# Optimization experiments

Hardware: AMD Instinct MI355X
Metric: run time of the kernel (lower is better)

Reference implementation:

```python
import jax, jax.numpy as jnp
import numpy as np

EPS = 2e-05
N_H_RDG = 9   # lifting scale grid: h_j = 2**j, j=0..8
N_H_CROP = 3  # group-conv scale support: offsets 0,1,2 (dyadic index shifts)


def _scaled_kernel(w, h):
    """Resample base kernel w [O, I, K] (taps on integers centered at 0) at
    coordinates x/h via linear interpolation -> [O, I, (K-1)*h+1], with the
    R+ Haar-measure normalization 1/h (psi_h(x) = psi(x/h)/h)."""
    K = w.shape[-1]
    Kh = (K - 1) * h + 1
    m = jnp.arange(K, dtype=jnp.float32) - K // 2
    x = (jnp.arange(Kh, dtype=jnp.float32) - Kh // 2) / h
    hat = jnp.maximum(0.0, 1.0 - jnp.abs(x[:, None] - m[None, :]))  # [Kh, K]
    return jnp.einsum('oim,xm->oix', w, hat) / h


def _conv1d_same(x, k):
    pad = (k.shape[-1] - 1) // 2
    return jax.lax.conv_general_dilated(
        x, k, window_strides=(1,), padding=[(pad, pad)],
        dimension_numbers=('NCH', 'OIH', 'NCH'))


def _pool_r1(x, stride):
    # max pool over the spatial (last) axis only: kernel 4, pad 1 each side
    return jax.lax.reduce_window(
        x, -jnp.inf, jax.lax.max,
        window_dimensions=(1, 1, 1, 4), window_strides=(1, 1, 1, stride),
        padding=((0, 0), (0, 0), (0, 0), (1, 1)))


def _bn(x, g, b):
    # BatchNorm2d over [B, C, H_scale, L], training-mode batch stats
    mu = jnp.mean(x, axis=(0, 2, 3), keepdims=True)
    var = jnp.var(x, axis=(0, 2, 3), keepdims=True)
    return (x - mu) * jax.lax.rsqrt(var + EPS) * g[None, :, None, None] + b[None, :, None, None]


def _forward(x, w1, w2, w3, g1, b1, g2, b2, g3, b3, fw1, fb1, fw2, fb2, fw3, fb3):
    B = x.shape[0]
    # --- c1: GConvRdG lifting, scales h_j = 2**j, j=0..8 ---
    out = jnp.stack([_conv1d_same(x, _scaled_kernel(w1, 2 ** j))
                     for j in range(N_H_RDG)], axis=2)      # [B,16,9,16]
    out = _bn(jax.nn.relu(_pool_r1(out, 2)), g1, b1)        # [B,16,9,8]
    # --- c2: GConvGG, h_crop=True: out scale j uses in scales j..j+2 ---
    O2, I2 = w2.shape[0], w2.shape[1]
    w2r = w2.reshape(O2, I2 * N_H_CROP, 3)
    H2 = out.shape[2] - (N_H_CROP - 1)  # 7
    out = jnp.stack([
        _conv1d_same(out[:, :, j:j + N_H_CROP, :].reshape(B, I2 * N_H_CROP, -1),
                     _scaled_kernel(w2r, 2 ** j))
        for j in range(H2)], axis=2)                        # [B,32,7,8]
    out = _bn(jax.nn.relu(_pool_r1(out, 2)), g2, b2)        # [B,32,7,4]
    # --- c3: GConvGG with 1x1 spatial kernel ---
    w3s = w3[:, :, :, 0]  # [64,32,3]
    H3 = out.shape[2] - (N_H_CROP - 1)  # 5
    out = jnp.stack([
        jnp.einsum('oik,bikl->bol', w3s, out[:, :, j:j + N_H_CROP, :]) / (2.0 ** j)
        for j in range(H3)], axis=2)                        # [B,64,5,4]
    out = _bn(jax.nn.relu(_pool_r1(out, 4)), g3, b3)        # [B,64,5,1]
    # --- MLP head (dropout is identity in eval) ---
    out = out.reshape(B, -1)                                # [B,320]
    out = out @ fw1.T + fb1
    out = out @ fw2.T + fb2
    return out @ fw3.T + fb3                                # [B,17]


def setup_inputs() -> dict:
    key = jax.random.key(0)
    ks = jax.random.split(key, 7)
    B = 4096
    x = jax.random.normal(ks[0], (B, 6, 16), dtype=jnp.float32)
    w1 = jax.random.normal(ks[1], (16, 6, 7), dtype=jnp.float32) * (6 * 7) ** -0.5
    w2 = jax.random.normal(ks[2], (32, 16, 3, 3), dtype=jnp.float32) * (16 * 3 * 3) ** -0.5
    w3 = jax.random.normal(ks[3], (64, 32, 3, 1), dtype=jnp.float32) * (32 * 3) ** -0.5
    fw1 = jax.random.normal(ks[4], (16, 320), dtype=jnp.float32) * 320 ** -0.5
    fw2 = jax.random.normal(ks[5], (16, 16), dtype=jnp.float32) * 16 ** -0.5
    fw3 = jax.random.normal(ks[6], (17, 16), dtype=jnp.float32) * 16 ** -0.5
    return {
        'x': x, 'w1': w1, 'w2': w2, 'w3': w3,
        'g1': jnp.ones(16), 'b1': jnp.zeros(16),
        'g2': jnp.ones(32), 'b2': jnp.zeros(32),
        'g3': jnp.ones(64), 'b3': jnp.zeros(64),
        'fw1': fw1, 'fb1': jnp.zeros(16),
        'fw2': fw2, 'fb2': jnp.zeros(16),
        'fw3': fw3, 'fb3': jnp.zeros(17),
    }


def reference(x, w1, w2, w3, g1, b1, g2, b2, g3, b3, fw1, fb1, fw2, fb2, fw3, fb3):
    return _forward(x, w1, w2, w3, g1, b1, g2, b2, g3, b3, fw1, fb1, fw2, fb2, fw3, fb3)
```

## Files before the change

kernel.cpp:

```cpp
#include <hip/hip_runtime.h>

#define EPS 2e-5f

using short8  = __attribute__((ext_vector_type(8))) short;
using floatx4 = __attribute__((ext_vector_type(4))) float;

static __device__ inline unsigned short f2bf(float f) {
    unsigned u = __float_as_uint(f);
    u += 0x7fffu + ((u >> 16) & 1u);
    return (unsigned short)(u >> 16);
}


__global__ void __launch_bounds__(256) k_setup(const float* __restrict__ w1,
                                               unsigned short* __restrict__ W1f,
                                               float* __restrict__ stats) {
    int gid = blockIdx.x * 256 + threadIdx.x;
    if (gid < 256) stats[gid] = 0.f;
    if (gid >= 221184) return;
    int j  = gid / 24576;
    int r  = gid % 24576;
    int T  = r / 1536;
    int r2 = r % 1536;
    int ks = r2 / 512;
    int r3 = r2 % 512;
    int lane = r3 >> 3, e = r3 & 7;
    int n  = T * 16 + (lane & 15);
    int kk = ks * 32 + (lane >> 4) * 8 + e;
    int o = n >> 4, t = n & 15;
    int i = kk >> 4, s = kk & 15;
    int h = 1 << j;
    int d = s - t;
    float val = 0.f;
    if (d >= -3 * h && d <= 3 * h) {
        float df = (float)d / (float)h;
        #pragma unroll
        for (int m = 0; m < 7; ++m) {
            float hat = fmaxf(0.f, 1.f - fabsf(df - (float)(m - 3)));
            val += w1[(o * 6 + i) * 7 + m] * hat;
        }
        val /= (float)h;
    }
    W1f[gid] = f2bf(val);
}

__global__ void __launch_bounds__(256) k1(const float* __restrict__ x,
                                          const unsigned short* __restrict__ W1f,
                                          unsigned short* __restrict__ p1,
                                          float* __restrict__ stats1) {
    int j    = blockIdx.y;
    int wav  = threadIdx.x >> 6;
    int lane = threadIdx.x & 63;
    int msub = wav & 1, nh = wav >> 1;
    int mt   = blockIdx.x * 2 + msub;
    int quad = lane >> 4, l15 = lane & 15;
    floatx4 z = {0.f, 0.f, 0.f, 0.f};
    floatx4 acc[8];
    #pragma unroll
    for (int T = 0; T < 8; ++T) acc[T] = z;
    const float* xr = x + (size_t)(mt * 16 + l15) * 96;
    const short8* Bj = (const short8*)W1f + (size_t)(j * 16) * 3 * 64;
    #pragma unroll
    for (int ks = 0; ks < 3; ++ks) {
        int k0 = ks * 32 + quad * 8;
        floatx4 v0 = *(const floatx4*)(xr + k0);
        floatx4 v1 = *(const floatx4*)(xr + k0 + 4);
        short8 a;
        #pragma unroll
        for (int e = 0; e < 4; ++e) {
            a[e]     = (short)f2bf(v0[e]);
            a[e + 4] = (short)f2bf(v1[e]);
        }
        #pragma unroll
        for (int T = 0; T < 8; ++T) {
            short8 b = Bj[((nh * 8 + T) * 3 + ks) * 64 + lane];
            acc[T] = __builtin_amdgcn_mfma_f32_16x16x32_bf16(a, b, acc[T], 0, 0, 0);
        }
    }
    __shared__ float ls[32];
    if (threadIdx.x < 32) ls[threadIdx.x] = 0.f;
    __syncthreads();
    int mbase = mt * 16 + quad * 4;
    int tp = l15;
    bool act = tp < 8;
    int tpe = tp & 7;
    int base = lane & 48;
    int c0 = base + max(2 * tpe - 1, 0);
    int c1 = base + 2 * tpe;
    int c2 = base + 2 * tpe + 1;
    int c3 = base + min(2 * tpe + 2, 15);
    #pragma unroll
    for (int T = 0; T < 8; ++T) {
        int o = nh * 8 + T;
        float psum = 0.f, pss = 0.f;
        #pragma unroll
        for (int r = 0; r < 4; ++r) {
            float v  = acc[T][r];
            float mx = fmaxf(fmaxf(__shfl(v, c0, 64), __shfl(v, c1, 64)),
                             fmaxf(__shfl(v, c2, 64), __shfl(v, c3, 64)));
            mx = fmaxf(mx, 0.f);
            if (act) {
                p1[(size_t)(mbase + r) * 1152 + o * 72 + j * 8 + tp] = f2bf(mx);
                psum += mx; pss += mx * mx;
            }
        }
        #pragma unroll
        for (int m = 32; m >= 1; m >>= 1) {
            psum += __shfl_xor(psum, m, 64);
            pss  += __shfl_xor(pss,  m, 64);
        }
        if (lane == 0) {
            atomicAdd(&ls[o], psum);
            atomicAdd(&ls[16 + o], pss);
        }
    }
    __syncthreads();
    if (threadIdx.x < 16) {
        atomicAdd(&stats1[threadIdx.x], ls[threadIdx.x]);
        atomicAdd(&stats1[16 + threadIdx.x], ls[16 + threadIdx.x]);
    }
}

__global__ void __launch_bounds__(384) k_bias(const float* __restrict__ w2,
                                              const float* __restrict__ g1,
                                              const float* __restrict__ b1,
                                              const float* __restrict__ stats1,
                                              unsigned short* __restrict__ W2f,
                                              float* __restrict__ bias2,
                                              float invN1) {
    int blk = blockIdx.x;
    int j   = blk >> 8;
    int col = blk & 255;
    int o = col >> 3, t = col & 7;
    int k = threadIdx.x;
    int ic = k >> 3, s = k & 7;
    int i = ic / 3, c = ic % 3;
    float mu  = stats1[i] * invN1;
    float var = stats1[16 + i] * invN1 - mu * mu;
    float rsg = rsqrtf(var + EPS);
    float a1  = g1[i] * rsg;
    float d1  = b1[i] - mu * a1;
    int h = 1 << j;
    int d = s - t;
    float raw = 0.f;
    if (d >= -h && d <= h) {
        float df = (float)d / (float)h;
        #pragma unroll
        for (int m = 0; m < 3; ++m) {
            float hat = fmaxf(0.f, 1.f - fabsf(df - (float)(m - 1)));
            raw += w2[((o * 16 + i) * 3 + c) * 3 + m] * hat;
        }
        raw /= (float)h;
    }
    {
        int T    = col >> 4;
        int lane = (col & 15) + ((k >> 3) & 3) * 16;
        int ks   = k >> 5;
        int e    = k & 7;
        W2f[(((size_t)(j * 16 + T) * 12 + ks) * 64 + lane) * 8 + e] = f2bf(raw * a1);
    }
    __shared__ float red[384];
    red[k] = raw * d1;
    __syncthreads();
    if (k < 128) red[k] += red[k + 128] + red[k + 256];
    __syncthreads();
    for (int st = 64; st >= 1; st >>= 1) {
        if (k < st) red[k] += red[k + st];
        __syncthreads();
    }
    if (k == 0) bias2[j * 256 + col] = red[0];
}

__global__ void __launch_bounds__(256) k2(const unsigned short* __restrict__ p1,
                                          const unsigned short* __restrict__ W2f,
                                          const float* __restrict__ bias2,
                                          unsigned short* __restrict__ p2s,
                                          float* __restrict__ stats2,
                                          int B) {
    int j    = blockIdx.y;
    int wav  = threadIdx.x >> 6;
    int lane = threadIdx.x & 63;
    int nh   = wav & 1, mp = wav >> 1;
    int m0   = blockIdx.x * 64 + mp * 32;
    int quad = lane >> 4, l15 = lane & 15;
    floatx4 z = {0.f, 0.f, 0.f, 0.f};
    floatx4 acc[2][8];
    #pragma unroll
    for (int mi = 0; mi < 2; ++mi)
        #pragma unroll
        for (int T = 0; T < 8; ++T) acc[mi][T] = z;
    const short8* Bj = (const short8*)W2f + (size_t)(j * 16) * 12 * 64;
    const unsigned short* Arow0 = p1 + (size_t)(m0 + l15) * 1152;
    const unsigned short* Arow1 = Arow0 + 16 * 1152;
    #pragma unroll
    for (int ks = 0; ks < 12; ++ks) {
        int k0 = ks * 32 + quad * 8;
        int i  = k0 / 24;
        int c  = (k0 - i * 24) >> 3;
        int off = i * 72 + (j + c) * 8;
        short8 a0 = *(const short8*)(Arow0 + off);
        short8 a1 = *(const short8*)(Arow1 + off);
        #pragma unroll
        for (int T = 0; T < 8; ++T) {
            short8 b = Bj[((nh * 8 + T) * 12 + ks) * 64 + lane];
            acc[0][T] = __builtin_amdgcn_mfma_f32_16x16x32_bf16(a0, b, acc[0][T], 0, 0, 0);
            acc[1][T] = __builtin_amdgcn_mfma_f32_16x16x32_bf16(a1, b, acc[1][T], 0, 0, 0);
        }
    }
    __shared__ float ls[64];
    if (threadIdx.x < 64) ls[threadIdx.x] = 0.f;
    __syncthreads();
    int tp  = lane & 7;
    bool act = tp < 4;
    int tpe = tp & 3;
    int base = lane & 56;
    int c0 = base + max(2 * tpe - 1, 0);
    int c1 = base + 2 * tpe;
    int c2 = base + 2 * tpe + 1;
    int c3 = base + min(2 * tpe + 2, 7);
    #pragma unroll
    for (int T = 0; T < 8; ++T) {
        int n = (nh * 8 + T) * 16 + l15;
        int o = n >> 3;
        float bias = bias2[j * 256 + n];
        float psum = 0.f, pss = 0.f;
        #pragma unroll
        for (int mi = 0; mi < 2; ++mi) {
            int mbase = m0 + mi * 16 + quad * 4;
            #pragma unroll
            for (int r = 0; r < 4; ++r) {
                float v  = acc[mi][T][r] + bias;
                float mx = fmaxf(fmaxf(__shfl(v, c0, 64), __shfl(v, c1, 64)),
                                 fmaxf(__shfl(v, c2, 64), __shfl(v, c3, 64)));
                mx = fmaxf(mx, 0.f);
                if (act) {
                    p2s[(((size_t)j * 4 + tp) * B + mbase + r) * 32 + o] = f2bf(mx);
                    psum += mx; pss += mx * mx;
                }
            }
        }
        #pragma unroll
        for (int m = 0; m < 5; ++m) {
            int msk = (m < 3) ? (1 << m) : (1 << (m + 1));
            psum += __shfl_xor(psum, msk, 64);
            pss  += __shfl_xor(pss,  msk, 64);
        }
        if (lane == 0 || lane == 8) {
            int oo = (nh * 8 + T) * 2 + (lane >> 3);
            atomicAdd(&ls[oo], psum);
            atomicAdd(&ls[32 + oo], pss);
        }
    }
    __syncthreads();
    if (threadIdx.x < 32) {
        atomicAdd(&stats2[threadIdx.x], ls[threadIdx.x]);
        atomicAdd(&stats2[32 + threadIdx.x], ls[32 + threadIdx.x]);
    }
}

__global__ void __launch_bounds__(256) k3(const unsigned short* __restrict__ p2s,
                                          const float* __restrict__ w3,
                                          const float* __restrict__ g2,
                                          const float* __restrict__ b2,
                                          const float* __restrict__ stats2,
                                          float* __restrict__ act3,
                                          float* __restrict__ stats3,
                                          float invN2, int B) {
    int j    = blockIdx.y;
    int wav  = threadIdx.x >> 6;
    int lane = threadIdx.x & 63;
    int msub = wav & 1, nh = wav >> 1;
    int m0   = (blockIdx.x * 2 + msub) * 16;
    int quad = lane >> 4, l15 = lane & 15;
    __shared__ float a2s[32], d2s[32], bias3s[64], ls[128];
    __shared__ unsigned short W3s[6144];
    if (threadIdx.x < 128) ls[threadIdx.x] = 0.f;
    if (threadIdx.x < 32) {
        int i = threadIdx.x;
        float mu  = stats2[i] * invN2;
        float var = stats2[32 + i] * invN2 - mu * mu;
        float rsg = rsqrtf(var + EPS);
        a2s[i] = g2[i] * rsg;
        d2s[i] = b2[i] - mu * a2s[i];
    }
    __syncthreads();
    for (int idx = threadIdx.x; idx < 6144; idx += 256) {
        int e  = idx & 7;
        int ln = (idx >> 3) & 63;
        int fs = idx >> 9;
        int Tg = fs / 3, ks = fs % 3;
        int n = Tg * 16 + (ln & 15);
        int i = (ln >> 4) * 8 + e;
        W3s[idx] = f2bf(w3[n * 96 + i * 3 + ks] * a2s[i]);
    }
    if (threadIdx.x < 64) {
        float s = 0.f;
        for (int i = 0; i < 32; ++i)
            #pragma unroll
            for (int kk = 0; kk < 3; ++kk)
                s = fmaf(w3[threadIdx.x * 96 + i * 3 + kk], d2s[i], s);
        bias3s[threadIdx.x] = s;
    }
    __syncthreads();
    short8 bf[2][3];
    #pragma unroll
    for (int T = 0; T < 2; ++T)
        #pragma unroll
        for (int ks = 0; ks < 3; ++ks)
            bf[T][ks] = *(const short8*)&W3s[(((nh * 2 + T) * 3 + ks) * 64 + lane) * 8];
    floatx4 z = {0.f, 0.f, 0.f, 0.f};
    floatx4 acc[2][3];
    #pragma unroll
    for (int T = 0; T < 2; ++T)
        #pragma unroll
        for (int l = 0; l < 3; ++l) acc[T][l] = z;
    #pragma unroll
    for (int ks = 0; ks < 3; ++ks) {
        int jj = j + ks;
        #pragma unroll
        for (int l = 0; l < 3; ++l) {
            const short8* ap =
                (const short8*)(p2s + ((size_t)(jj * 4 + l) * B + m0 + l15) * 32) + quad;
            short8 a = *ap;
            #pragma unroll
            for (int T = 0; T < 2; ++T)
                acc[T][l] = __builtin_amdgcn_mfma_f32_16x16x32_bf16(a, bf[T][ks],
                                                                    acc[T][l], 0, 0, 0);
        }
    }
    float inv = 1.f / (float)(1 << j);
    int mbase = m0 + quad * 4;
    #pragma unroll
    for (int T = 0; T < 2; ++T) {
        int col = nh * 32 + T * 16 + l15;
        float bias = bias3s[col];
        float psum = 0.f, pss = 0.f;
        #pragma unroll
        for (int r = 0; r < 4; ++r) {
            float v = fmaxf(fmaxf(acc[T][0][r], acc[T][1][r]), acc[T][2][r]);
            v = fmaxf((v + bias) * inv, 0.f);
            act3[(size_t)(mbase + r) * 320 + col * 5 + j] = v;
            psum += v; pss += v * v;
        }
        psum += __shfl_xor(psum, 16, 64); pss += __shfl_xor(pss, 16, 64);
        psum += __shfl_xor(psum, 32, 64); pss += __shfl_xor(pss, 32, 64);
        if (quad == 0) {
            atomicAdd(&ls[col], psum);
            atomicAdd(&ls[64 + col], pss);
        }
    }
    __syncthreads();
    if (threadIdx.x < 64) {
        atomicAdd(&stats3[threadIdx.x], ls[threadIdx.x]);
        atomicAdd(&stats3[64 + threadIdx.x], ls[64 + threadIdx.x]);
    }
}

__global__ void __launch_bounds__(128) k4(const float* __restrict__ act3,
                                          const float* __restrict__ g3,
                                          const float* __restrict__ b3,
                                          const float* __restrict__ stats3,
                                          const float* __restrict__ fw1,
                                          const float* __restrict__ fb1,
                                          const float* __restrict__ fw2,
                                          const float* __restrict__ fb2,
                                          const float* __restrict__ fw3,
                                          const float* __restrict__ fb3,
                                          float* __restrict__ out,
                                          float invN3) {
    __shared__ float a3s[64], d3s[64];
    __shared__ unsigned short W1s[5120];
    __shared__ float fw2s[256], fw3s[272], fb2s[16], fb3s[17], fb1f[16];
    __shared__ float hbuf[2][16][17];
    int tid = threadIdx.x;
    if (tid < 64) {
        float mu  = stats3[tid] * invN3;
        float var = stats3[64 + tid] * invN3 - mu * mu;
        float rsg = rsqrtf(var + EPS);
        a3s[tid] = g3[tid] * rsg;
        d3s[tid] = b3[tid] - mu * a3s[tid];
    }
    __syncthreads();
    for (int idx = tid; idx < 5120; idx += 128) {
        int e  = idx & 7;
        int ln = (idx >> 3) & 63;
        int ks = idx >> 9;
        int n  = ln & 15;
        int k  = ks * 32 + (ln >> 4) * 8 + e;
        W1s[idx] = f2bf(fw1[n * 320 + k] * a3s[k / 5]);
    }
    for (int idx = tid; idx < 256; idx += 128) fw2s[idx] = fw2[idx];
    for (int idx = tid; idx < 272; idx += 128) fw3s[idx] = fw3[idx];
    if (tid < 16) fb2s[tid] = fb2[tid];
    if (tid < 17) fb3s[tid] = fb3[tid];
    if (tid < 16) {
        float s = fb1[tid];
        for (int o = 0; o < 64; ++o) {
            float dd = d3s[o];
            #pragma unroll
            for (int jj = 0; jj < 5; ++jj)
                s = fmaf(fw1[tid * 320 + o * 5 + jj], dd, s);
        }
        fb1f[tid] = s;
    }
    __syncthreads();
    int wav = tid >> 6, lane = tid & 63;
    int quad = lane >> 4, l15 = lane & 15;
    int mt = blockIdx.x * 2 + wav;
    const float* ar = act3 + (size_t)(mt * 16 + l15) * 320;
    floatx4 acc = {0.f, 0.f, 0.f, 0.f};
    #pragma unroll
    for (int ks = 0; ks < 10; ++ks) {
        int k0 = ks * 32 + quad * 8;
        floatx4 v0 = *(const floatx4*)(ar + k0);
        floatx4 v1 = *(const floatx4*)(ar + k0 + 4);
        short8 a;
        #pragma unroll
        for (int e = 0; e < 4; ++e) {
            a[e]     = (short)f2bf(v0[e]);
            a[e + 4] = (short)f2bf(v1[e]);
        }
        short8 b = *(const short8*)&W1s[(ks * 64 + lane) * 8];
        acc = __builtin_amdgcn_mfma_f32_16x16x32_bf16(a, b, acc, 0, 0, 0);
    }
    #pragma unroll
    for (int r = 0; r < 4; ++r)
        hbuf[wav][quad * 4 + r][l15] = acc[r] + fb1f[l15];
    __syncthreads();
    if (lane < 16) {
        int row = l15;
        float hv[16];
        #pragma unroll
        for (int n = 0; n < 16; ++n) hv[n] = hbuf[wav][row][n];
        float h2[16];
        #pragma unroll
        for (int f2 = 0; f2 < 16; ++f2) {
            float s = fb2s[f2];
            #pragma unroll
            for (int n = 0; n < 16; ++n) s = fmaf(fw2s[f2 * 16 + n], hv[n], s);
            h2[f2] = s;
        }
        float* orow = out + (size_t)(mt * 16 + row) * 17;
        #pragma unroll
        for (int f3 = 0; f3 < 17; ++f3) {
            float s = fb3s[f3];
            #pragma unroll
            for (int n = 0; n < 16; ++n) s = fmaf(fw3s[f3 * 16 + n], h2[n], s);
            orow[f3] = s;
        }
    }
}

extern "C" void kernel_launch(void* const* d_in, const int* in_sizes, int n_in,
                              void* d_out, int out_size, void* d_ws, size_t ws_size,
                              hipStream_t stream) {
    (void)n_in; (void)out_size; (void)ws_size;
    const float* x   = (const float*)d_in[0];
    const float* w1  = (const float*)d_in[1];
    const float* w2  = (const float*)d_in[2];
    const float* w3  = (const float*)d_in[3];
    const float* g1  = (const float*)d_in[4];
    const float* b1  = (const float*)d_in[5];
    const float* g2  = (const float*)d_in[6];
    const float* b2  = (const float*)d_in[7];
    const float* g3  = (const float*)d_in[8];
    const float* b3  = (const float*)d_in[9];
    const float* fw1 = (const float*)d_in[10];
    const float* fb1 = (const float*)d_in[11];
    const float* fw2 = (const float*)d_in[12];
    const float* fb2 = (const float*)d_in[13];
    const float* fw3 = (const float*)d_in[14];
    const float* fb3 = (const float*)d_in[15];
    float* out = (float*)d_out;

    int B = in_sizes[0] / 96;

    char* wsb = (char*)d_ws;
    float*          stats  = (float*)wsb;
    unsigned short* W1f    = (unsigned short*)(wsb + 1024);
    unsigned short* W2f    = W1f + 221184;
    float*          bias2  = (float*)(W2f + 688128);
    unsigned short* p1     = (unsigned short*)(bias2 + 1792);
    unsigned short* p2s    = p1 + (size_t)B * 1152;
    float*          act3   = (float*)(p2s + (size_t)B * 896);

    float* stats1 = stats;
    float* stats2 = stats + 32;
    float* stats3 = stats + 96;

    float invN1 = 1.f / (float)(B * 72);
    float invN2 = 1.f / (float)(B * 28);
    float invN3 = 1.f / (float)(B * 5);

    k_setup<<<864, 256, 0, stream>>>(w1, W1f, stats);
    k1<<<dim3(B / 32, 9), 256, 0, stream>>>(x, W1f, p1, stats1);
    k_bias<<<7 * 256, 384, 0, stream>>>(w2, g1, b1, stats1, W2f, bias2, invN1);
    k2<<<dim3(B / 64, 7), 256, 0, stream>>>(p1, W2f, bias2, p2s, stats2, B);
    k3<<<dim3(B / 32, 5), 256, 0, stream>>>(p2s, w3, g2, b2, stats2, act3, stats3,
                                            invN2, B);
    k4<<<B / 32, 128, 0, stream>>>(act3, g3, b3, stats3, fw1, fb1, fw2, fb2, fw3, fb3,
                                   out, invN3);
}
```

Baseline: 204.1 us.

## Restage epilogues through shared memory and re-layout intermediates for vector stores

The per-element shuffle pooling and scattered 2-byte global stores in k1/k2 are replaced by staging MFMA accumulators in LDS, doing the max-pool per thread, and writing packed short8 rows. The p1, p2s and act3 intermediates get scale-major layouts, with act3 now stored as bf16 instead of fp32. k3 is restructured so the BN-folded weights become the A operand and are built in registers rather than staged in LDS. k4 runs at 16 rows per 64-thread block and reads the bf16 act3 directly. The aim is to cut global memory traffic and uncoalesced stores, at the cost of more LDS use and extra barriers.

```diff
diff --git a/kernel.cpp b/kernel.cpp
--- a/kernel.cpp
+++ b/kernel.cpp
@@ -12,9 +12,9 @@
 }
 
 
-__global__ void __launch_bounds__(256) k_setup(const float* __restrict__ w1,
-                                               unsigned short* __restrict__ W1f,
-                                               float* __restrict__ stats) {
+__global__ void __launch_bounds__(256) kS(const float* __restrict__ w1,
+                                          unsigned short* __restrict__ W1f,
+                                          float* __restrict__ stats) {
     int gid = blockIdx.x * 256 + threadIdx.x;
     if (gid < 256) stats[gid] = 0.f;
     if (gid >= 221184) return;
@@ -24,9 +24,9 @@
     int r2 = r % 1536;
     int ks = r2 / 512;
     int r3 = r2 % 512;
-    int lane = r3 >> 3, e = r3 & 7;
-    int n  = T * 16 + (lane & 15);
-    int kk = ks * 32 + (lane >> 4) * 8 + e;
+    int ln = r3 >> 3, e = r3 & 7;
+    int n  = T * 16 + (ln & 15);
+    int kk = ks * 32 + (ln >> 4) * 8 + e;
     int o = n >> 4, t = n & 15;
     int i = kk >> 4, s = kk & 15;
     int h = 1 << j;
@@ -47,18 +47,18 @@
 __global__ void __launch_bounds__(256) k1(const float* __restrict__ x,
                                           const unsigned short* __restrict__ W1f,
                                           unsigned short* __restrict__ p1,
-                                          float* __restrict__ stats1) {
-    int j    = blockIdx.y;
-    int wav  = threadIdx.x >> 6;
-    int lane = threadIdx.x & 63;
+                                          float* __restrict__ stats1, int B) {
+    __shared__ float z[32 * 276];
+    __shared__ float lsS[256], lsQ[256];
+    int tid = threadIdx.x, j = blockIdx.y;
+    int wav = tid >> 6, lane = tid & 63;
+    int quad = lane >> 4, l15 = lane & 15;
     int msub = wav & 1, nh = wav >> 1;
-    int mt   = blockIdx.x * 2 + msub;
-    int quad = lane >> 4, l15 = lane & 15;
-    floatx4 z = {0.f, 0.f, 0.f, 0.f};
+    int b0 = blockIdx.x * 32;
     floatx4 acc[8];
     #pragma unroll
-    for (int T = 0; T < 8; ++T) acc[T] = z;
-    const float* xr = x + (size_t)(mt * 16 + l15) * 96;
+    for (int T = 0; T < 8; ++T) acc[T] = floatx4{0.f, 0.f, 0.f, 0.f};
+    const float* xr = x + (size_t)(b0 + msub * 16 + l15) * 96;
     const short8* Bj = (const short8*)W1f + (size_t)(j * 16) * 3 * 64;
     #pragma unroll
     for (int ks = 0; ks < 3; ++ks) {
@@ -77,47 +77,49 @@
             acc[T] = __builtin_amdgcn_mfma_f32_16x16x32_bf16(a, b, acc[T], 0, 0, 0);
         }
     }
-    __shared__ float ls[32];
-    if (threadIdx.x < 32) ls[threadIdx.x] = 0.f;
-    __syncthreads();
-    int mbase = mt * 16 + quad * 4;
-    int tp = l15;
-    bool act = tp < 8;
-    int tpe = tp & 7;
-    int base = lane & 48;
-    int c0 = base + max(2 * tpe - 1, 0);
-    int c1 = base + 2 * tpe;
-    int c2 = base + 2 * tpe + 1;
-    int c3 = base + min(2 * tpe + 2, 15);
     #pragma unroll
     for (int T = 0; T < 8; ++T) {
-        int o = nh * 8 + T;
-        float psum = 0.f, pss = 0.f;
-        #pragma unroll
-        for (int r = 0; r < 4; ++r) {
-            float v  = acc[T][r];
-            float mx = fmaxf(fmaxf(__shfl(v, c0, 64), __shfl(v, c1, 64)),
-                             fmaxf(__shfl(v, c2, 64), __shfl(v, c3, 64)));
-            mx = fmaxf(mx, 0.f);
-            if (act) {
-                p1[(size_t)(mbase + r) * 1152 + o * 72 + j * 8 + tp] = f2bf(mx);
-                psum += mx; pss += mx * mx;
-            }
-        }
-        #pragma unroll
-        for (int m = 32; m >= 1; m >>= 1) {
-            psum += __shfl_xor(psum, m, 64);
-            pss  += __shfl_xor(pss,  m, 64);
-        }
-        if (lane == 0) {
-            atomicAdd(&ls[o], psum);
-            atomicAdd(&ls[16 + o], pss);
-        }
-    }
-    __syncthreads();
-    if (threadIdx.x < 16) {
-        atomicAdd(&stats1[threadIdx.x], ls[threadIdx.x]);
-        atomicAdd(&stats1[16 + threadIdx.x], ls[16 + threadIdx.x]);
+        int col = (nh * 8 + T) * 16 + l15;
+        int rb  = msub * 16 + quad * 4;
+        #pragma unroll
+        for (int r = 0; r < 4; ++r) z[(rb + r) * 276 + col] = acc[T][r];
+    }
+    __syncthreads();
+    float psum = 0.f, pss = 0.f;
+    #pragma unroll
+    for (int i = 0; i < 2; ++i) {
+        int u = tid + 256 * i;
+        int row = u >> 4, o = u & 15;
+        const float* zr = &z[row * 276 + o * 16];
+        floatx4 q0 = ((const floatx4*)zr)[0];
+        floatx4 q1 = ((const floatx4*)zr)[1];
+        floatx4 q2 = ((const floatx4*)zr)[2];
+        floatx4 q3 = ((const floatx4*)zr)[3];
+        float t[16] = {q0[0], q0[1], q0[2], q0[3], q1[0], q1[1], q1[2], q1[3],
+                       q2[0], q2[1], q2[2], q2[3], q3[0], q3[1], q3[2], q3[3]};
+        short8 pk;
+        #pragma unroll
+        for (int tp = 0; tp < 8; ++tp) {
+            int lo = (tp == 0) ? 0 : 2 * tp - 1;
+            int hi = (tp == 7) ? 15 : 2 * tp + 2;
+            float m = t[lo];
+            for (int tt = lo + 1; tt <= hi; ++tt) m = fmaxf(m, t[tt]);
+            m = fmaxf(m, 0.f);
+            pk[tp] = (short)f2bf(m);
+            psum += m; pss += m * m;
+        }
+        *(short8*)(p1 + ((size_t)j * B + b0 + row) * 128 + o * 8) = pk;
+    }
+    lsS[(tid & 15) * 16 + (tid >> 4)] = psum;
+    lsQ[(tid & 15) * 16 + (tid >> 4)] = pss;
+    __syncthreads();
+    if (tid < 32) {
+        int o = tid & 15;
+        const float* src = (tid < 16) ? lsS : lsQ;
+        float s = 0.f;
+        #pragma unroll
+        for (int g = 0; g < 16; ++g) s += src[o * 16 + g];
+        atomicAdd(&stats1[(tid < 16 ? 0 : 16) + o], s);
     }
 }
 
@@ -175,31 +177,28 @@
                                           const unsigned short* __restrict__ W2f,
                                           const float* __restrict__ bias2,
                                           unsigned short* __restrict__ p2s,
-                                          float* __restrict__ stats2,
-                                          int B) {
-    int j    = blockIdx.y;
-    int wav  = threadIdx.x >> 6;
-    int lane = threadIdx.x & 63;
-    int nh   = wav & 1, mp = wav >> 1;
-    int m0   = blockIdx.x * 64 + mp * 32;
+                                          float* __restrict__ stats2, int B) {
+    __shared__ float z[32 * 260];
+    __shared__ unsigned short pt[4][64][40];
+    __shared__ float lsS[512], lsQ[512];
+    int tid = threadIdx.x, j = blockIdx.y;
+    int wav = tid >> 6, lane = tid & 63;
     int quad = lane >> 4, l15 = lane & 15;
-    floatx4 z = {0.f, 0.f, 0.f, 0.f};
+    int nh = wav & 1, mp = wav >> 1;
+    int b0 = blockIdx.x * 64, m0 = b0 + mp * 32;
     floatx4 acc[2][8];
     #pragma unroll
     for (int mi = 0; mi < 2; ++mi)
         #pragma unroll
-        for (int T = 0; T < 8; ++T) acc[mi][T] = z;
+        for (int T = 0; T < 8; ++T) acc[mi][T] = floatx4{0.f, 0.f, 0.f, 0.f};
     const short8* Bj = (const short8*)W2f + (size_t)(j * 16) * 12 * 64;
-    const unsigned short* Arow0 = p1 + (size_t)(m0 + l15) * 1152;
-    const unsigned short* Arow1 = Arow0 + 16 * 1152;
     #pragma unroll
     for (int ks = 0; ks < 12; ++ks) {
-        int k0 = ks * 32 + quad * 8;
-        int i  = k0 / 24;
-        int c  = (k0 - i * 24) >> 3;
-        int off = i * 72 + (j + c) * 8;
-        short8 a0 = *(const short8*)(Arow0 + off);
-        short8 a1 = *(const short8*)(Arow1 + off);
+        int icq = ks * 4 + quad;
+        int i = icq / 3, c = icq - i * 3;
+        const unsigned short* ap = p1 + ((size_t)(j + c) * B + m0 + l15) * 128 + i * 8;
+        short8 a0 = *(const short8*)ap;
+        short8 a1 = *(const short8*)(ap + 2048);
         #pragma unroll
         for (int T = 0; T < 8; ++T) {
             short8 b = Bj[((nh * 8 + T) * 12 + ks) * 64 + lane];
@@ -207,54 +206,73 @@
             acc[1][T] = __builtin_amdgcn_mfma_f32_16x16x32_bf16(a1, b, acc[1][T], 0, 0, 0);
         }
     }
-    __shared__ float ls[64];
-    if (threadIdx.x < 64) ls[threadIdx.x] = 0.f;
-    __syncthreads();
-    int tp  = lane & 7;
-    bool act = tp < 4;
-    int tpe = tp & 3;
-    int base = lane & 56;
-    int c0 = base + max(2 * tpe - 1, 0);
-    int c1 = base + 2 * tpe;
-    int c2 = base + 2 * tpe + 1;
-    int c3 = base + min(2 * tpe + 2, 7);
-    #pragma unroll
-    for (int T = 0; T < 8; ++T) {
-        int n = (nh * 8 + T) * 16 + l15;
-        int o = n >> 3;
-        float bias = bias2[j * 256 + n];
-        float psum = 0.f, pss = 0.f;
-        #pragma unroll
-        for (int mi = 0; mi < 2; ++mi) {
-            int mbase = m0 + mi * 16 + quad * 4;
+    float biasv[8];
+    #pragma unroll
+    for (int T = 0; T < 8; ++T) biasv[T] = bias2[j * 256 + (nh * 8 + T) * 16 + l15];
+    float psum[2] = {0.f, 0.f}, pss[2] = {0.f, 0.f};
+    for (int pass = 0; pass < 2; ++pass) {
+        __syncthreads();
+        if (mp == pass) {
             #pragma unroll
-            for (int r = 0; r < 4; ++r) {
-                float v  = acc[mi][T][r] + bias;
-                float mx = fmaxf(fmaxf(__shfl(v, c0, 64), __shfl(v, c1, 64)),
-                                 fmaxf(__shfl(v, c2, 64), __shfl(v, c3, 64)));
-                mx = fmaxf(mx, 0.f);
-                if (act) {
-                    p2s[(((size_t)j * 4 + tp) * B + mbase + r) * 32 + o] = f2bf(mx);
-                    psum += mx; pss += mx * mx;
+            for (int T = 0; T < 8; ++T) {
+                int col = (nh * 8 + T) * 16 + l15;
+                #pragma unroll
+                for (int mi = 0; mi < 2; ++mi) {
+                    int rb = mi * 16 + quad * 4;
+                    #pragma unroll
+                    for (int r = 0; r < 4; ++r)
+                        z[(rb + r) * 260 + col] = acc[mi][T][r] + biasv[T];
                 }
             }
         }
-        #pragma unroll
-        for (int m = 0; m < 5; ++m) {
-            int msk = (m < 3) ? (1 << m) : (1 << (m + 1));
-            psum += __shfl_xor(psum, msk, 64);
-            pss  += __shfl_xor(pss,  msk, 64);
-        }
-        if (lane == 0 || lane == 8) {
-            int oo = (nh * 8 + T) * 2 + (lane >> 3);
-            atomicAdd(&ls[oo], psum);
-            atomicAdd(&ls[32 + oo], pss);
-        }
-    }
-    __syncthreads();
-    if (threadIdx.x < 32) {
-        atomicAdd(&stats2[threadIdx.x], ls[threadIdx.x]);
-        atomicAdd(&stats2[32 + threadIdx.x], ls[32 + threadIdx.x]);
+        __syncthreads();
+        #pragma unroll
+        for (int i2 = 0; i2 < 2; ++i2) {
+            int u = tid + 256 * i2;
+            int opr = u & 15, row = u >> 4;
+            const float* zr = &z[row * 260 + opr * 16];
+            floatx4 q0 = ((const floatx4*)zr)[0];
+            floatx4 q1 = ((const floatx4*)zr)[1];
+            floatx4 q2 = ((const floatx4*)zr)[2];
+            floatx4 q3 = ((const floatx4*)zr)[3];
+            float ta[8] = {q0[0], q0[1], q0[2], q0[3], q1[0], q1[1], q1[2], q1[3]};
+            float tb[8] = {q2[0], q2[1], q2[2], q2[3], q3[0], q3[1], q3[2], q3[3]};
+            int rowg = pass * 32 + row;
+            #pragma unroll
+            for (int tp = 0; tp < 4; ++tp) {
+                int lo = (tp == 0) ? 0 : 2 * tp - 1;
+                int hi = (tp == 3) ? 7 : 2 * tp + 2;
+                float m0v = ta[lo], m1v = tb[lo];
+                for (int tt = lo + 1; tt <= hi; ++tt) {
+                    m0v = fmaxf(m0v, ta[tt]); m1v = fmaxf(m1v, tb[tt]);
+                }
+                m0v = fmaxf(m0v, 0.f); m1v = fmaxf(m1v, 0.f);
+                psum[0] += m0v; pss[0] += m0v * m0v;
+                psum[1] += m1v; pss[1] += m1v * m1v;
+                unsigned pk = (unsigned)f2bf(m0v) | ((unsigned)f2bf(m1v) << 16);
+                *(unsigned*)&pt[tp][rowg][opr * 2] = pk;
+            }
+        }
+    }
+    {
+        int o0 = 2 * (tid & 15), g = tid >> 4;
+        lsS[o0 * 16 + g] = psum[0]; lsS[(o0 + 1) * 16 + g] = psum[1];
+        lsQ[o0 * 16 + g] = pss[0];  lsQ[(o0 + 1) * 16 + g] = pss[1];
+    }
+    __syncthreads();
+    #pragma unroll
+    for (int tp = 0; tp < 4; ++tp) {
+        int oct = tid & 3, row = (tid >> 2) & 63;
+        *(short8*)(p2s + ((size_t)(j * 4 + tp) * B + b0 + row) * 32 + oct * 8) =
+            *(const short8*)&pt[tp][row][oct * 8];
+    }
+    if (tid < 64) {
+        int o = tid & 31;
+        const float* src = (tid < 32) ? lsS : lsQ;
+        float s = 0.f;
+        #pragma unroll
+        for (int g = 0; g < 16; ++g) s += src[o * 16 + g];
+        atomicAdd(&stats2[(tid < 32 ? 0 : 32) + o], s);
     }
 }
 
@@ -263,175 +281,164 @@
                                           const float* __restrict__ g2,
                                           const float* __restrict__ b2,
                                           const float* __restrict__ stats2,
-                                          float* __restrict__ act3,
+                                          unsigned short* __restrict__ act3,
                                           float* __restrict__ stats3,
                                           float invN2, int B) {
-    int j    = blockIdx.y;
-    int wav  = threadIdx.x >> 6;
-    int lane = threadIdx.x & 63;
-    int msub = wav & 1, nh = wav >> 1;
-    int m0   = (blockIdx.x * 2 + msub) * 16;
+    __shared__ float a2s[32], d2s[32];
+    __shared__ unsigned short atile[32][72];
+    __shared__ float lsS[1024], lsQ[1024];
+    int tid = threadIdx.x, j = blockIdx.y, b0 = blockIdx.x * 32;
+    int og = tid >> 6, lane = tid & 63;
     int quad = lane >> 4, l15 = lane & 15;
-    __shared__ float a2s[32], d2s[32], bias3s[64], ls[128];
-    __shared__ unsigned short W3s[6144];
-    if (threadIdx.x < 128) ls[threadIdx.x] = 0.f;
-    if (threadIdx.x < 32) {
-        int i = threadIdx.x;
-        float mu  = stats2[i] * invN2;
-        float var = stats2[32 + i] * invN2 - mu * mu;
-        float rsg = rsqrtf(var + EPS);
-        a2s[i] = g2[i] * rsg;
-        d2s[i] = b2[i] - mu * a2s[i];
-    }
-    __syncthreads();
-    for (int idx = threadIdx.x; idx < 6144; idx += 256) {
+    if (tid < 32) {
+        float mu  = stats2[tid] * invN2;
+        float var = stats2[32 + tid] * invN2 - mu * mu;
+        float rs  = rsqrtf(var + EPS);
+        a2s[tid] = g2[tid] * rs;
+        d2s[tid] = b2[tid] - mu * a2s[tid];
+    }
+    __syncthreads();
+    int o = og * 16 + l15;
+    float biasacc = 0.f;
+    short8 af[3];
+    #pragma unroll
+    for (int kf = 0; kf < 3; ++kf) {
+        short8 v;
+        #pragma unroll
+        for (int e = 0; e < 8; ++e) {
+            int i = quad * 8 + e;
+            float raw = w3[o * 96 + i * 3 + kf];
+            v[e] = (short)f2bf(raw * a2s[i]);
+            biasacc = fmaf(raw, d2s[i], biasacc);
+        }
+        af[kf] = v;
+    }
+    biasacc += __shfl_xor(biasacc, 16, 64);
+    biasacc += __shfl_xor(biasacc, 32, 64);
+    float brow[4];
+    #pragma unroll
+    for (int r = 0; r < 4; ++r) brow[r] = __shfl(biasacc, quad * 4 + r, 64);
+    float inv = 1.f / (float)(1 << j);
+    float psum[4] = {0.f, 0.f, 0.f, 0.f}, pss[4] = {0.f, 0.f, 0.f, 0.f};
+    #pragma unroll
+    for (int bt = 0; bt < 2; ++bt) {
+        int bb = b0 + bt * 16;
+        floatx4 aL0 = {0.f, 0.f, 0.f, 0.f};
+        floatx4 aL1 = {0.f, 0.f, 0.f, 0.f};
+        floatx4 aL2 = {0.f, 0.f, 0.f, 0.f};
+        #pragma unroll
+        for (int c = 0; c < 3; ++c) {
+            const unsigned short* base =
+                p2s + ((size_t)((j + c) * 4) * B + bb + l15) * 32 + quad * 8;
+            short8 f0 = *(const short8*)base;
+            short8 f1 = *(const short8*)(base + (size_t)B * 32);
+            short8 f2v = *(const short8*)(base + (size_t)2 * B * 32);
+            aL0 = __builtin_amdgcn_mfma_f32_16x16x32_bf16(af[c], f0, aL0, 0, 0, 0);
+            aL1 = __builtin_amdgcn_mfma_f32_16x16x32_bf16(af[c], f1, aL1, 0, 0, 0);
+            aL2 = __builtin_amdgcn_mfma_f32_16x16x32_bf16(af[c], f2v, aL2, 0, 0, 0);
+        }
+        #pragma unroll
+        for (int r = 0; r < 4; ++r) {
+            float vm = fmaxf(fmaxf(aL0[r], aL1[r]), aL2[r]);
+            float v  = fmaxf((vm + brow[r]) * inv, 0.f);
+            atile[bt * 16 + l15][og * 16 + quad * 4 + r] = f2bf(v);
+            psum[r] += v; pss[r] += v * v;
+        }
+    }
+    #pragma unroll
+    for (int r = 0; r < 4; ++r) {
+        lsS[(og * 16 + quad * 4 + r) * 16 + l15] = psum[r];
+        lsQ[(og * 16 + quad * 4 + r) * 16 + l15] = pss[r];
+    }
+    __syncthreads();
+    {
+        int row = tid >> 3, oct = tid & 7;
+        *(short8*)(act3 + ((size_t)j * B + b0 + row) * 64 + oct * 8) =
+            *(const short8*)&atile[row][oct * 8];
+    }
+    if (tid < 128) {
+        int oo = tid & 63;
+        const float* src = (tid < 64) ? lsS : lsQ;
+        float s = 0.f;
+        #pragma unroll
+        for (int g = 0; g < 16; ++g) s += src[oo * 16 + g];
+        atomicAdd(&stats3[(tid < 64 ? 0 : 64) + oo], s);
+    }
+}
+
+__global__ void __launch_bounds__(64) k4(const unsigned short* __restrict__ act3,
+                                         const float* __restrict__ g3,
+                                         const float* __restrict__ b3,
+                                         const float* __restrict__ stats3,
+                                         const float* __restrict__ fw1,
+                                         const float* __restrict__ fb1,
+                                         const float* __restrict__ fw2,
+                                         const float* __restrict__ fb2,
+                                         const float* __restrict__ fw3,
+                                         const float* __restrict__ fb3,
+                                         float* __restrict__ out,
+                                         float invN3, int B) {
+    __shared__ float a3s[64], d3s[64];
+    __shared__ unsigned short W1s[5120];
+    __shared__ float fw2s[256], fw3s[272], fb2s[16], fb3s[17], fb1f[16], tmp[4][16];
+    __shared__ float hbuf[16][17];
+    int tid = threadIdx.x, lane = tid;
+    int quad = lane >> 4, l15 = lane & 15;
+    {
+        float mu  = stats3[tid] * invN3;
+        float var = stats3[64 + tid] * invN3 - mu * mu;
+        float rs  = rsqrtf(var + EPS);
+        a3s[tid] = g3[tid] * rs;
+        d3s[tid] = b3[tid] - mu * a3s[tid];
+    }
+    __syncthreads();
+    #pragma unroll 4
+    for (int k = 0; k < 80; ++k) {
+        int idx = tid + 64 * k;
         int e  = idx & 7;
         int ln = (idx >> 3) & 63;
         int fs = idx >> 9;
-        int Tg = fs / 3, ks = fs % 3;
-        int n = Tg * 16 + (ln & 15);
-        int i = (ln >> 4) * 8 + e;
-        W3s[idx] = f2bf(w3[n * 96 + i * 3 + ks] * a2s[i]);
-    }
-    if (threadIdx.x < 64) {
-        float s = 0.f;
-        for (int i = 0; i < 32; ++i)
-            #pragma unroll
-            for (int kk = 0; kk < 3; ++kk)
-                s = fmaf(w3[threadIdx.x * 96 + i * 3 + kk], d2s[i], s);
-        bias3s[threadIdx.x] = s;
-    }
-    __syncthreads();
-    short8 bf[2][3];
-    #pragma unroll
-    for (int T = 0; T < 2; ++T)
-        #pragma unroll
-        for (int ks = 0; ks < 3; ++ks)
-            bf[T][ks] = *(const short8*)&W3s[(((nh * 2 + T) * 3 + ks) * 64 + lane) * 8];
-    floatx4 z = {0.f, 0.f, 0.f, 0.f};
-    floatx4 acc[2][3];
-    #pragma unroll
-    for (int T = 0; T < 2; ++T)
-        #pragma unroll
-        for (int l = 0; l < 3; ++l) acc[T][l] = z;
-    #pragma unroll
-    for (int ks = 0; ks < 3; ++ks) {
-        int jj = j + ks;
-        #pragma unroll
-        for (int l = 0; l < 3; ++l) {
-            const short8* ap =
-                (const short8*)(p2s + ((size_t)(jj * 4 + l) * B + m0 + l15) * 32) + quad;
-            short8 a = *ap;
-            #pragma unroll
-            for (int T = 0; T < 2; ++T)
-                acc[T][l] = __builtin_amdgcn_mfma_f32_16x16x32_bf16(a, bf[T][ks],
-                                                                    acc[T][l], 0, 0, 0);
-        }
-    }
-    float inv = 1.f / (float)(1 << j);
-    int mbase = m0 + quad * 4;
-    #pragma unroll
-    for (int T = 0; T < 2; ++T) {
-        int col = nh * 32 + T * 16 + l15;
-        float bias = bias3s[col];
-        float psum = 0.f, pss = 0.f;
-        #pragma unroll
-        for (int r = 0; r < 4; ++r) {
-            float v = fmaxf(fmaxf(acc[T][0][r], acc[T][1][r]), acc[T][2][r]);
-            v = fmaxf((v + bias) * inv, 0.f);
-            act3[(size_t)(mbase + r) * 320 + col * 5 + j] = v;
-            psum += v; pss += v * v;
-        }
-        psum += __shfl_xor(psum, 16, 64); pss += __shfl_xor(pss, 16, 64);
-        psum += __shfl_xor(psum, 32, 64); pss += __shfl_xor(pss, 32, 64);
-        if (quad == 0) {
-            atomicAdd(&ls[col], psum);
-            atomicAdd(&ls[64 + col], pss);
-        }
-    }
-    __syncthreads();
-    if (threadIdx.x < 64) {
-        atomicAdd(&stats3[threadIdx.x], ls[threadIdx.x]);
-        atomicAdd(&stats3[64 + threadIdx.x], ls[64 + threadIdx.x]);
-    }
-}
-
-__global__ void __launch_bounds__(128) k4(const float* __restrict__ act3,
-                                          const float* __restrict__ g3,
-                                          const float* __restrict__ b3,
-                                          const float* __restrict__ stats3,
-                                          const float* __restrict__ fw1,
-                                          const float* __restrict__ fb1,
-                                          const float* __restrict__ fw2,
-                                          const float* __restrict__ fb2,
-                                          const float* __restrict__ fw3,
-                                          const float* __restrict__ fb3,
-                                          float* __restrict__ out,
-                                          float invN3) {
-    __shared__ float a3s[64], d3s[64];
-    __shared__ unsigned short W1s[5120];
-    __shared__ float fw2s[256], fw3s[272], fb2s[16], fb3s[17], fb1f[16];
-    __shared__ float hbuf[2][16][17];
-    int tid = threadIdx.x;
-    if (tid < 64) {
-        float mu  = stats3[tid] * invN3;
-        float var = stats3[64 + tid] * invN3 - mu * mu;
-        float rsg = rsqrtf(var + EPS);
-        a3s[tid] = g3[tid] * rsg;
-        d3s[tid] = b3[tid] - mu * a3s[tid];
-    }
-    __syncthreads();
-    for (int idx = tid; idx < 5120; idx += 128) {
-        int e  = idx & 7;
-        int ln = (idx >> 3) & 63;
-        int ks = idx >> 9;
-        int n  = ln & 15;
-        int k  = ks * 32 + (ln >> 4) * 8 + e;
-        W1s[idx] = f2bf(fw1[n * 320 + k] * a3s[k / 5]);
-    }
-    for (int idx = tid; idx < 256; idx += 128) fw2s[idx] = fw2[idx];
-    for (int idx = tid; idx < 272; idx += 128) fw3s[idx] = fw3[idx];
+        int jj = fs >> 1, ks = fs & 1;
+        int n = ln & 15;
+        int oo = ks * 32 + (ln >> 4) * 8 + e;
+        W1s[idx] = f2bf(fw1[n * 320 + oo * 5 + jj] * a3s[oo]);
+    }
+    #pragma unroll
+    for (int k = 0; k < 4; ++k) fw2s[tid + 64 * k] = fw2[tid + 64 * k];
+    for (int idx = tid; idx < 272; idx += 64) fw3s[idx] = fw3[idx];
     if (tid < 16) fb2s[tid] = fb2[tid];
     if (tid < 17) fb3s[tid] = fb3[tid];
-    if (tid < 16) {
-        float s = fb1[tid];
-        for (int o = 0; o < 64; ++o) {
-            float dd = d3s[o];
-            #pragma unroll
-            for (int jj = 0; jj < 5; ++jj)
-                s = fmaf(fw1[tid * 320 + o * 5 + jj], dd, s);
-        }
-        fb1f[tid] = s;
-    }
-    __syncthreads();
-    int wav = tid >> 6, lane = tid & 63;
-    int quad = lane >> 4, l15 = lane & 15;
-    int mt = blockIdx.x * 2 + wav;
-    const float* ar = act3 + (size_t)(mt * 16 + l15) * 320;
+    {
+        int f = tid & 15, ch = tid >> 4;
+        float s = 0.f;
+        for (int u = 0; u < 80; ++u) {
+            int n = ch * 80 + u;
+            s = fmaf(fw1[f * 320 + n], d3s[n / 5], s);
+        }
+        tmp[ch][f] = s;
+    }
+    __syncthreads();
+    if (tid < 16) fb1f[tid] = fb1[tid] + tmp[0][tid] + tmp[1][tid] + tmp[2][tid] + tmp[3][tid];
+    __syncthreads();
+    int mt = blockIdx.x;
     floatx4 acc = {0.f, 0.f, 0.f, 0.f};
     #pragma unroll
-    for (int ks = 0; ks < 10; ++ks) {
-        int k0 = ks * 32 + quad * 8;
-        floatx4 v0 = *(const floatx4*)(ar + k0);
-        floatx4 v1 = *(const floatx4*)(ar + k0 + 4);
-        short8 a;
-        #pragma unroll
-        for (int e = 0; e < 4; ++e) {
-            a[e]     = (short)f2bf(v0[e]);
-            a[e + 4] = (short)f2bf(v1[e]);
-        }
-        short8 b = *(const short8*)&W1s[(ks * 64 + lane) * 8];
-        acc = __builtin_amdgcn_mfma_f32_16x16x32_bf16(a, b, acc, 0, 0, 0);
-    }
-    #pragma unroll
-    for (int r = 0; r < 4; ++r)
-        hbuf[wav][quad * 4 + r][l15] = acc[r] + fb1f[l15];
+    for (int jj = 0; jj < 5; ++jj)
+        #pragma unroll
+        for (int ks = 0; ks < 2; ++ks) {
+            short8 a = *(const short8*)(act3 +
+                ((size_t)jj * B + mt * 16 + l15) * 64 + ks * 32 + quad * 8);
+            short8 b = *(const short8*)&W1s[((jj * 2 + ks) * 64 + lane) * 8];
+            acc = __builtin_amdgcn_mfma_f32_16x16x32_bf16(a, b, acc, 0, 0, 0);
+        }
+    #pragma unroll
+    for (int r = 0; r < 4; ++r) hbuf[quad * 4 + r][l15] = acc[r] + fb1f[l15];
     __syncthreads();
     if (lane < 16) {
         int row = l15;
         float hv[16];
         #pragma unroll
-        for (int n = 0; n < 16; ++n) hv[n] = hbuf[wav][row][n];
+        for (int n = 0; n < 16; ++n) hv[n] = hbuf[row][n];
         float h2[16];
         #pragma unroll
         for (int f2 = 0; f2 < 16; ++f2) {
@@ -476,13 +483,13 @@
     int B = in_sizes[0] / 96;
 
     char* wsb = (char*)d_ws;
-    float*          stats  = (float*)wsb;
-    unsigned short* W1f    = (unsigned short*)(wsb + 1024);
-    unsigned short* W2f    = W1f + 221184;
-    float*          bias2  = (float*)(W2f + 688128);
-    unsigned short* p1     = (unsigned short*)(bias2 + 1792);
-    unsigned short* p2s    = p1 + (size_t)B * 1152;
-    float*          act3   = (float*)(p2s + (size_t)B * 896);
+    float*          stats = (float*)wsb;
+    unsigned short* W1f   = (unsigned short*)(wsb + 1024);
+    unsigned short* W2f   = W1f + 221184;
+    float*          bias2 = (float*)(W2f + 688128);
+    unsigned short* p1    = (unsigned short*)(bias2 + 1792);
+    unsigned short* p2s   = p1 + (size_t)9 * B * 128;
+    unsigned short* act3  = p2s + (size_t)28 * B * 32;
 
     float* stats1 = stats;
     float* stats2 = stats + 32;
@@ -492,12 +499,12 @@
     float invN2 = 1.f / (float)(B * 28);
     float invN3 = 1.f / (float)(B * 5);
 
-    k_setup<<<864, 256, 0, stream>>>(w1, W1f, stats);
-    k1<<<dim3(B / 32, 9), 256, 0, stream>>>(x, W1f, p1, stats1);
+    kS<<<864, 256, 0, stream>>>(w1, W1f, stats);
+    k1<<<dim3(B / 32, 9), 256, 0, stream>>>(x, W1f, p1, stats1, B);
     k_bias<<<7 * 256, 384, 0, stream>>>(w2, g1, b1, stats1, W2f, bias2, invN1);
     k2<<<dim3(B / 64, 7), 256, 0, stream>>>(p1, W2f, bias2, p2s, stats2, B);
     k3<<<dim3(B / 32, 5), 256, 0, stream>>>(p2s, w3, g2, b2, stats2, act3, stats3,
                                             invN2, B);
-    k4<<<B / 32, 128, 0, stream>>>(act3, g3, b3, stats3, fw1, fb1, fw2, fb2, fw3, fb3,
-                                   out, invN3);
-}
+    k4<<<B / 16, 64, 0, stream>>>(act3, g3, b3, stats3, fw1, fb1, fw2, fb2, fw3, fb3,
+                                  out, invN3, B);
+}
```

Result: faster. 178.2 us (-12.7%).
